# Kernel optimization log

Hardware: AMD Instinct MI355X
Metric: run time of the kernel (lower is better)

The kernel has to match this reference:

```python
import jax, jax.numpy as jnp
import numpy as np

V, Tb, D, H, L = 50257, 1024, 768, 12, 12
HS = D // H  # head size 64
DF = 4 * D   # MLP hidden 3072


def setup_inputs() -> dict:
    key = jax.random.key(0)
    ks = jax.random.split(key, 24)
    s = 0.02
    inp = {}
    inp['x'] = jax.random.randint(ks[0], (1, Tb), 0, V, dtype=jnp.int64)
    inp['wte'] = jax.random.normal(ks[1], (V, D), jnp.float32) * s
    inp['wpe'] = jax.random.normal(ks[2], (Tb, D), jnp.float32) * s
    # per-layer, per-head QKV linears, stacked: [L, H, D, HS]
    inp['Wq'] = jax.random.normal(ks[3], (L, H, D, HS), jnp.float32) * s
    inp['bq'] = jnp.zeros((L, H, HS), jnp.float32)
    inp['Wk'] = jax.random.normal(ks[4], (L, H, D, HS), jnp.float32) * s
    inp['bk'] = jnp.zeros((L, H, HS), jnp.float32)
    inp['Wv'] = jax.random.normal(ks[5], (L, H, D, HS), jnp.float32) * s
    inp['bv'] = jnp.zeros((L, H, HS), jnp.float32)
    inp['ln1_s'] = jnp.ones((L, D), jnp.float32)
    inp['ln1_b'] = jnp.zeros((L, D), jnp.float32)
    inp['W1'] = jax.random.normal(ks[6], (L, D, DF), jnp.float32) * s
    inp['b1'] = jnp.zeros((L, DF), jnp.float32)
    inp['W2'] = jax.random.normal(ks[7], (L, DF, D), jnp.float32) * s
    inp['b2'] = jnp.zeros((L, D), jnp.float32)
    inp['ln2_s'] = jnp.ones((L, D), jnp.float32)
    inp['ln2_b'] = jnp.zeros((L, D), jnp.float32)
    inp['lnf_s'] = jnp.ones((D,), jnp.float32)
    inp['lnf_b'] = jnp.zeros((D,), jnp.float32)
    inp['Wlm'] = jax.random.normal(ks[8], (D, V), jnp.float32) * s
    return inp


def _layernorm(x, scale, bias, eps=1e-5):
    mu = jnp.mean(x, axis=-1, keepdims=True)
    var = jnp.var(x, axis=-1, keepdims=True)
    return (x - mu) * jax.lax.rsqrt(var + eps) * scale + bias


def _gpt2_forward(x, wte, wpe, Wq, bq, Wk, bk, Wv, bv, ln1_s, ln1_b,
                  W1, b1, W2, b2, ln2_s, ln2_b, lnf_s, lnf_b, Wlm):
    B, T = x.shape
    h = wte[x] + wpe[jnp.arange(T)][None]  # [B, T, D]
    mask = jnp.tril(jnp.ones((T, T), jnp.bool_))
    for l in range(L):
        xn = _layernorm(h, ln1_s[l], ln1_b[l])
        # per-head linears, stacked -> [B, H, T, HS]
        q = jnp.einsum('btd,hde->bhte', xn, Wq[l]) + bq[l][None, :, None, :]
        k = jnp.einsum('btd,hde->bhte', xn, Wk[l]) + bk[l][None, :, None, :]
        v = jnp.einsum('btd,hde->bhte', xn, Wv[l]) + bv[l][None, :, None, :]
        # NOTE: original module does NOT scale scores by 1/sqrt(head_size)
        scores = jnp.einsum('bhte,bhse->bhts', q, k)
        scores = jnp.where(mask[None, None], scores, -jnp.inf)
        w = jax.nn.softmax(scores, axis=-1)
        attn = jnp.einsum('bhts,bhse->bhte', w, v)
        attn = attn.transpose(0, 2, 1, 3).reshape(B, T, H * HS)
        h = h + attn  # residual (no output projection in original)
        xn2 = _layernorm(h, ln2_s[l], ln2_b[l])
        mlp = jnp.einsum('btd,df->btf', xn2, W1[l]) + b1[l]
        mlp = jax.nn.gelu(mlp, approximate=False)  # nn.GELU default = exact
        mlp = jnp.einsum('btf,fd->btd', mlp, W2[l]) + b2[l]
        h = h + mlp
    h = _layernorm(h, lnf_s, lnf_b)
    logits = jnp.einsum('btd,dv->btv', h, Wlm)  # lm_head, no bias
    return logits


def reference(x, wte, wpe, Wq, bq, Wk, bk, Wv, bv, ln1_s, ln1_b,
              W1, b1, W2, b2, ln2_s, ln2_b, lnf_s, lnf_b, Wlm):
    return _gpt2_forward(x, wte, wpe, Wq, bq, Wk, bk, Wv, bv, ln1_s, ln1_b,
                         W1, b1, W2, b2, ln2_s, ln2_b, lnf_s, lnf_b, Wlm)
```

## Files before the change

### kernel.cpp

```cpp
#include <hip/hip_runtime.h>
#include <math.h>

#define TLEN 1024
#define DM   768
#define NH   12
#define HSZ  64
#define DF_  3072
#define NL   12
#define VC   50257
#define VCP  50304
#define NPAN (VCP/128)

typedef __attribute__((ext_vector_type(8))) short bf16x8;
typedef __attribute__((ext_vector_type(4))) float f32x4;

__device__ __forceinline__ float gelu_exact(float x){
  return 0.5f * x * (1.0f + erff(x * 0.70710678118654752f));
}
__device__ __forceinline__ short f2bf(float f){
  union { float f; unsigned u; } x; x.f = f;
  unsigned r = x.u + 0x7fffu + ((x.u >> 16) & 1u);
  return (short)(r >> 16);
}
__device__ __forceinline__ void gl16(const void* g, void* l){
  __builtin_amdgcn_global_load_lds(
      (const __attribute__((address_space(1))) unsigned int*)g,
      (__attribute__((address_space(3))) unsigned int*)l, 16, 0, 0);
}

__global__ __launch_bounds__(256) void embedln_k(const int* __restrict__ x,
    const float* __restrict__ wte, const float* __restrict__ wpe,
    const float* __restrict__ sc, const float* __restrict__ bi,
    float* __restrict__ h, short* __restrict__ out)
{
  int w = threadIdx.x >> 6, lane = threadIdx.x & 63;
  int t = blockIdx.x * 4 + w;
  int tok = x[t];
  size_t off = (size_t)t * DM;
  float v[12];
  float s = 0.f, s2 = 0.f;
  #pragma unroll
  for (int i = 0; i < 12; i++){
    int c = lane + i * 64;
    float xv = wte[(size_t)tok * DM + c] + wpe[off + c];
    h[off + c] = xv;
    v[i] = xv; s += xv; s2 += xv * xv;
  }
  #pragma unroll
  for (int o = 32; o; o >>= 1){ s += __shfl_xor(s, o); s2 += __shfl_xor(s2, o); }
  float mu = s * (1.0f / DM);
  float var = s2 * (1.0f / DM) - mu * mu;
  float rs = rsqrtf(var + 1e-5f);
  #pragma unroll
  for (int i = 0; i < 12; i++){
    int c = lane + i * 64;
    out[off + c] = f2bf((v[i] - mu) * rs * sc[c] + bi[c]);
  }
}

__global__ __launch_bounds__(256) void ln_k(const float* __restrict__ in,
    const float* __restrict__ sc, const float* __restrict__ bi,
    short* __restrict__ out)
{
  int w = threadIdx.x >> 6, lane = threadIdx.x & 63;
  int row = blockIdx.x * 4 + w;
  const float* r = in + (size_t)row * DM;
  float v[12];
  float s = 0.f, s2 = 0.f;
  #pragma unroll
  for (int i = 0; i < 12; i++){
    float xv = r[lane + i * 64];
    v[i] = xv; s += xv; s2 += xv * xv;
  }
  #pragma unroll
  for (int o = 32; o; o >>= 1){ s += __shfl_xor(s, o); s2 += __shfl_xor(s2, o); }
  float mu  = s * (1.0f / DM);
  float var = s2 * (1.0f / DM) - mu * mu;
  float rs  = rsqrtf(var + 1e-5f);
  short* o = out + (size_t)row * DM;
  #pragma unroll
  for (int i = 0; i < 12; i++){
    int c = lane + i * 64;
    o[c] = f2bf((v[i] - mu) * rs * sc[c] + bi[c]);
  }
}

__global__ __launch_bounds__(256) void redln_k(float* __restrict__ h,
    const float* __restrict__ p0, const float* __restrict__ p1,
    const float* __restrict__ bias,
    const float* __restrict__ sc, const float* __restrict__ bi,
    short* __restrict__ out)
{
  int w = threadIdx.x >> 6, lane = threadIdx.x & 63;
  int row = blockIdx.x * 4 + w;
  size_t off = (size_t)row * DM;
  float v[12];
  float s = 0.f, s2 = 0.f;
  #pragma unroll
  for (int i = 0; i < 12; i++){
    int c = lane + i * 64;
    float xv = h[off + c] + p0[off + c] + p1[off + c] + bias[c];
    h[off + c] = xv;
    v[i] = xv; s += xv; s2 += xv * xv;
  }
  #pragma unroll
  for (int o = 32; o; o >>= 1){ s += __shfl_xor(s, o); s2 += __shfl_xor(s2, o); }
  float mu  = s * (1.0f / DM);
  float var = s2 * (1.0f / DM) - mu * mu;
  float rs  = rsqrtf(var + 1e-5f);
  #pragma unroll
  for (int i = 0; i < 12; i++){
    int c = lane + i * 64;
    out[off + c] = f2bf((v[i] - mu) * rs * sc[c] + bi[c]);
  }
}

__global__ __launch_bounds__(256) void tc_k(const float* __restrict__ in,
    short* __restrict__ out, int K, int N, int ntiles, int per_mat,
    size_t in_stride, size_t out_stride)
{
  __shared__ short sh[64][65];
  int b = blockIdx.x;
  int l = b / per_mat, r = b - l * per_mat;
  int nt = r % ntiles, kt = r / ntiles;
  const float* ip = in + (size_t)l * in_stride;
  short* op = out + (size_t)l * out_stride;
  int n0 = nt * 64, k0 = kt * 64;
  int tid = threadIdx.x;
  if ((N & 3) == 0){
    #pragma unroll
    for (int it = 0; it < 4; it++){
      int idx = it * 256 + tid;
      int k = idx >> 4, n4 = (idx & 15) * 4;
      float4 v = *(const float4*)(ip + (size_t)(k0 + k) * N + n0 + n4);
      sh[k][n4+0] = f2bf(v.x); sh[k][n4+1] = f2bf(v.y);
      sh[k][n4+2] = f2bf(v.z); sh[k][n4+3] = f2bf(v.w);
    }
  } else {
    #pragma unroll
    for (int it = 0; it < 16; it++){
      int idx = it * 256 + tid;
      int k = idx >> 6, n = idx & 63;
      float v = (n0 + n < N) ? ip[(size_t)(k0 + k) * N + n0 + n] : 0.f;
      sh[k][n] = f2bf(v);
    }
  }
  __syncthreads();
  #pragma unroll
  for (int it = 0; it < 2; it++){
    int n = it * 32 + (tid >> 3);
    int kc = (tid & 7) * 8;
    bf16x8 v;
    #pragma unroll
    for (int u = 0; u < 8; u++) v[u] = sh[kc + u][n];
    *(bf16x8*)(op + (size_t)(n0 + n) * K + k0 + kc) = v;
  }
}

__global__ __launch_bounds__(256) void tcqkv_k(const float* __restrict__ Wq,
    const float* __restrict__ Wk, const float* __restrict__ Wv,
    short* __restrict__ out)
{
  __shared__ short sh[64][65];
  int b = blockIdx.x;
  int l = b / 144; int r = b - l * 144;
  int h = r / 12, kt = r - h * 12;
  int tid = threadIdx.x;
  for (int p = 0; p < 3; p++){
    const float* ip = (p == 0 ? Wq : p == 1 ? Wk : Wv)
                      + ((size_t)(l * NH + h) * DM + kt * 64) * 64;
    if (p) __syncthreads();
    #pragma unroll
    for (int it = 0; it < 4; it++){
      int idx = it * 256 + tid;
      int k = idx >> 4, e4 = (idx & 15) * 4;
      float4 v = *(const float4*)(ip + (size_t)k * 64 + e4);
      sh[k][e4+0] = f2bf(v.x); sh[k][e4+1] = f2bf(v.y);
      sh[k][e4+2] = f2bf(v.z); sh[k][e4+3] = f2bf(v.w);
    }
    __syncthreads();
    short* op = out + (size_t)l * 2304 * DM + (size_t)(p * DM + h * 64) * DM;
    #pragma unroll
    for (int it = 0; it < 2; it++){
      int e = it * 32 + (tid >> 3);
      int kc = (tid & 7) * 8;
      bf16x8 v;
      #pragma unroll
      for (int u = 0; u < 8; u++) v[u] = sh[kc + u][e];
      *(bf16x8*)(op + (size_t)e * DM + kt * 64 + kc) = v;
    }
  }
}

template<int MODE, int FI, int FJ>
__global__ __launch_bounds__(256) void mg_k(
    const short* __restrict__ A, const short* __restrict__ Bt,
    const float* __restrict__ b0, const float* __restrict__ b1,
    const float* __restrict__ b2,
    void* __restrict__ C0, void* __restrict__ C1, void* __restrict__ C2)
{
  constexpr int LDA    = (MODE == 2) ? DF_ : DM;
  constexpr int BM     = FI * 32;
  constexpr int BN     = FJ * 32;
  constexpr int ABYTES = BM * 64 * 2;
  constexpr int BBYTES = BN * 64 * 2;
  __shared__ __align__(16) char lds[2 * (ABYTES + BBYTES)];

  int tid = threadIdx.x;
  int wid = tid >> 6, lane = tid & 63;
  int l15 = lane & 15, l4 = lane >> 4;
  int wr = wid >> 1, wc = wid & 1;

  int m0, n0;
  if (MODE == 3){
    int xcd = blockIdx.x & 7, slot = blockIdx.x >> 3;
    int nb = xcd + 8 * (slot >> 3);
    if (nb >= NPAN) return;
    m0 = (slot & 7) * BM;
    n0 = nb * BN;
  } else {
    m0 = blockIdx.x * BM;
    n0 = blockIdx.y * BN;
  }
  int kbeg = (MODE == 2) ? blockIdx.z * (DF_ / 2) : 0;
  int nk   = ((MODE == 2) ? DF_ / 2 : LDA) / 64;

  f32x4 acc[FI][FJ] = {};
  int wbase = (tid & ~63) * 16;

  auto stage = [&](int k0, int b){
    char* ab = lds + b * ABYTES;
    char* bb = lds + 2 * ABYTES + b * BBYTES;
    #pragma unroll
    for (int ia = 0; ia < FI; ia++){
      int d = ia * 256 + tid;
      int row = d >> 3, gs = (d & 7) ^ (row & 7);
      gl16(A + (size_t)(m0 + row) * LDA + k0 + gs * 8, ab + ia * 4096 + wbase);
    }
    #pragma unroll
    for (int ib = 0; ib < FJ; ib++){
      int d = ib * 256 + tid;
      int row = d >> 3, gs = (d & 7) ^ (row & 7);
      gl16(Bt + (size_t)(n0 + row) * LDA + k0 + gs * 8, bb + ib * 4096 + wbase);
    }
  };

  stage(kbeg, 0);
  int cur = 0;
  for (int t = 0; t < nk; ++t){
    int k0 = kbeg + t * 64;
    if (t + 1 < nk){
      stage(k0 + 64, cur ^ 1);
      if constexpr (FI + FJ == 4) asm volatile("s_waitcnt vmcnt(4)" ::: "memory");
      else                        asm volatile("s_waitcnt vmcnt(8)" ::: "memory");
    } else {
      asm volatile("s_waitcnt vmcnt(0)" ::: "memory");
    }
    __builtin_amdgcn_s_barrier();
    __builtin_amdgcn_sched_barrier(0);

    char* ab = lds + cur * ABYTES;
    char* bb = lds + 2 * ABYTES + cur * BBYTES;
    #pragma unroll
    for (int kk = 0; kk < 2; kk++){
      bf16x8 af[FI], bfr[FJ];
      #pragma unroll
      for (int i = 0; i < FI; i++){
        int row = wr * (FI * 16) + i * 16 + l15;
        af[i] = *(const bf16x8*)(ab + row * 128 + (((kk * 4 + l4) ^ (row & 7)) * 16));
      }
      #pragma unroll
      for (int j = 0; j < FJ; j++){
        int row = wc * (FJ * 16) + j * 16 + l15;
        bfr[j] = *(const bf16x8*)(bb + row * 128 + (((kk * 4 + l4) ^ (row & 7)) * 16));
      }
      #pragma unroll
      for (int i = 0; i < FI; i++)
        #pragma unroll
        for (int j = 0; j < FJ; j++)
          acc[i][j] = __builtin_amdgcn_mfma_f32_16x16x32_bf16(af[i], bfr[j], acc[i][j], 0, 0, 0);
    }
    __builtin_amdgcn_sched_barrier(0);
    __builtin_amdgcn_s_barrier();
    cur ^= 1;
  }

  #pragma unroll
  for (int i = 0; i < FI; i++){
    int rowb = m0 + wr * (FI * 16) + i * 16 + l4 * 4;
    #pragma unroll
    for (int j = 0; j < FJ; j++){
      int col = n0 + wc * (FJ * 16) + j * 16 + l15;
      if (MODE == 0){
        int p = col / DM, within = col - p * DM;
        const float* bp = (p == 0) ? b0 : (p == 1) ? b1 : b2;
        float bb2 = bp[within];
        int hd = within >> 6, e = within & 63;
        if (p < 2){
          short* dst = (short*)((p == 0) ? C0 : C1);
          #pragma unroll
          for (int r = 0; r < 4; r++)
            dst[((size_t)hd * TLEN + rowb + r) * 64 + e] = f2bf(acc[i][j][r] + bb2);
        } else {
          short4 pk;
          pk.x = f2bf(acc[i][j][0] + bb2); pk.y = f2bf(acc[i][j][1] + bb2);
          pk.z = f2bf(acc[i][j][2] + bb2); pk.w = f2bf(acc[i][j][3] + bb2);
          *(short4*)((short*)C2 + ((size_t)hd * 64 + e) * TLEN + rowb) = pk;
        }
      } else if (MODE == 1){
        #pragma unroll
        for (int r = 0; r < 4; r++)
          ((short*)C0)[(size_t)(rowb + r) * DF_ + col] =
              f2bf(gelu_exact(acc[i][j][r] + b0[col]));
      } else if (MODE == 2){
        float* dst = (float*)((blockIdx.z == 0) ? C0 : C1);
        #pragma unroll
        for (int r = 0; r < 4; r++)
          dst[(size_t)(rowb + r) * DM + col] = acc[i][j][r];
      } else {
        if (col < VC){
          #pragma unroll
          for (int r = 0; r < 4; r++)
            ((float*)C0)[(size_t)(rowb + r) * VC + col] = acc[i][j][r];
        }
      }
    }
  }
}

__global__ __launch_bounds__(256) void attn_k(const short* __restrict__ q,
    const short* __restrict__ k, const short* __restrict__ vt,
    float* __restrict__ h)
{
  __shared__ short P_lds[4][16][72];
  int tid = threadIdx.x;
  int wid = tid >> 6, lane = tid & 63;
  int l15 = lane & 15, l4 = lane >> 4;
  int head = blockIdx.x >> 4, qt = blockIdx.x & 15;
  int qb = qt * 64 + wid * 16;

  const short* qh = q  + (size_t)head * TLEN * 64;
  const short* kh = k  + (size_t)head * TLEN * 64;
  const short* vh = vt + (size_t)head * 64 * TLEN;

  bf16x8 qf[2];
  qf[0] = *(const bf16x8*)(qh + (size_t)(qb + l15) * 64 + l4 * 8);
  qf[1] = *(const bf16x8*)(qh + (size_t)(qb + l15) * 64 + 32 + l4 * 8);

  f32x4 O[4] = {};
  float mrow[4] = {-3e38f, -3e38f, -3e38f, -3e38f};
  float lrow[4] = {0.f, 0.f, 0.f, 0.f};

  for (int kv0 = 0; kv0 <= qb + 15; kv0 += 64){
    f32x4 S[4] = {};
    #pragma unroll
    for (int kk = 0; kk < 2; kk++){
      #pragma unroll
      for (int j = 0; j < 4; j++){
        bf16x8 kf = *(const bf16x8*)(kh + (size_t)(kv0 + j*16 + l15) * 64
                                     + kk*32 + l4*8);
        S[j] = __builtin_amdgcn_mfma_f32_16x16x32_bf16(qf[kk], kf, S[j], 0, 0, 0);
      }
    }
    if (kv0 + 63 > qb){
      #pragma unroll
      for (int j = 0; j < 4; j++){
        int kvc = kv0 + j*16 + l15;
        #pragma unroll
        for (int r = 0; r < 4; r++)
          if (kvc > qb + l4*4 + r) S[j][r] = -3e38f;
      }
    }
    #pragma unroll
    for (int r = 0; r < 4; r++){
      float mx = fmaxf(fmaxf(S[0][r], S[1][r]), fmaxf(S[2][r], S[3][r]));
      #pragma unroll
      for (int off = 1; off < 16; off <<= 1) mx = fmaxf(mx, __shfl_xor(mx, off));
      float mn = fmaxf(mrow[r], mx);
      float corr = __expf(mrow[r] - mn);
      mrow[r] = mn;
      float sm = 0.f;
      #pragma unroll
      for (int j = 0; j < 4; j++){
        float p = __expf(S[j][r] - mn);
        S[j][r] = p; sm += p;
      }
      #pragma unroll
      for (int off = 1; off < 16; off <<= 1) sm += __shfl_xor(sm, off);
      lrow[r] = lrow[r] * corr + sm;
      #pragma unroll
      for (int j = 0; j < 4; j++) O[j][r] *= corr;
    }
    #pragma unroll
    for (int j = 0; j < 4; j++)
      #pragma unroll
      for (int r = 0; r < 4; r++)
        P_lds[wid][l4*4 + r][j*16 + l15] = f2bf(S[j][r]);
    #pragma unroll
    for (int kk = 0; kk < 2; kk++){
      bf16x8 pa = *(const bf16x8*)(&P_lds[wid][l15][kk*32 + l4*8]);
      #pragma unroll
      for (int jd = 0; jd < 4; jd++){
        bf16x8 vf = *(const bf16x8*)(vh + (size_t)(jd*16 + l15) * TLEN
                                     + kv0 + kk*32 + l4*8);
        O[jd] = __builtin_amdgcn_mfma_f32_16x16x32_bf16(pa, vf, O[jd], 0, 0, 0);
      }
    }
  }

  #pragma unroll
  for (int r = 0; r < 4; r++){
    float inv = 1.0f / lrow[r];
    int t = qb + l4*4 + r;
    #pragma unroll
    for (int jd = 0; jd < 4; jd++){
      int d = head * 64 + jd*16 + l15;
      h[(size_t)t * DM + d] += O[jd][r] * inv;
    }
  }
}

extern "C" void kernel_launch(void* const* d_in, const int* in_sizes, int n_in,
                              void* d_out, int out_size, void* d_ws, size_t ws_size,
                              hipStream_t stream)
{
  const int*   x    = (const int*)  d_in[0];
  const float* wte  = (const float*)d_in[1];
  const float* wpe  = (const float*)d_in[2];
  const float* Wq   = (const float*)d_in[3];
  const float* bq   = (const float*)d_in[4];
  const float* Wk   = (const float*)d_in[5];
  const float* bk   = (const float*)d_in[6];
  const float* Wv   = (const float*)d_in[7];
  const float* bv   = (const float*)d_in[8];
  const float* ln1s = (const float*)d_in[9];
  const float* ln1b = (const float*)d_in[10];
  const float* W1   = (const float*)d_in[11];
  const float* b1   = (const float*)d_in[12];
  const float* W2   = (const float*)d_in[13];
  const float* b2   = (const float*)d_in[14];
  const float* ln2s = (const float*)d_in[15];
  const float* ln2b = (const float*)d_in[16];
  const float* lnfs = (const float*)d_in[17];
  const float* lnfb = (const float*)d_in[18];
  const float* Wlm  = (const float*)d_in[19];
  float* out = (float*)d_out;

  const size_t SZ_QKVT = (size_t)NL * 2304 * DM * 2;
  const size_t SZ_W1T  = (size_t)NL * DF_ * DM * 2;
  const size_t SZ_W2T  = (size_t)NL * DM * DF_ * 2;
  const size_t SZ_WLMT = (size_t)VCP * DM * 2;
  const size_t SZ_H    = (size_t)TLEN * DM * 4;
  const size_t SZ_BF   = (size_t)TLEN * DM * 2;

  char* ws = (char*)d_ws;
  short* wqkvT = (short*)ws;  ws += SZ_QKVT;
  short* w1T   = (short*)ws;  ws += SZ_W1T;
  short* w2T   = (short*)ws;  ws += SZ_W2T;
  short* wlmT  = (short*)ws;  ws += SZ_WLMT;
  float* h     = (float*)ws;  ws += SZ_H;
  short* qb    = (short*)ws;  ws += SZ_BF;
  short* kb    = (short*)ws;  ws += SZ_BF;
  short* vtb   = (short*)ws;  ws += SZ_BF;
  short* xnb   = (short*)ws;  ws += SZ_BF;
  short* mhb   = (short*)ws;  ws += (size_t)TLEN * DF_ * 2;
  float* p1    = (float*)ws;
  float* p0    = (float*)qb;

  tcqkv_k<<<NL*NH*12, 256, 0, stream>>>(Wq, Wk, Wv, wqkvT);
  tc_k<<<NL*48*12, 256, 0, stream>>>(W1, w1T, DM, DF_, 48, 576,
                                     (size_t)DM*DF_, (size_t)DM*DF_);
  tc_k<<<NL*12*48, 256, 0, stream>>>(W2, w2T, DF_, DM, 12, 576,
                                     (size_t)DM*DF_, (size_t)DM*DF_);
  tc_k<<<786*12, 256, 0, stream>>>(Wlm, wlmT, DM, VC, 786, 786*12, 0, 0);

  embedln_k<<<TLEN/4, 256, 0, stream>>>(x, wte, wpe, ln1s, ln1b, h, xnb);

  for (int l = 0; l < NL; ++l){
    mg_k<0,2,2><<<dim3(16,36), 256, 0, stream>>>(xnb, wqkvT + (size_t)l*2304*DM,
        bq + l*DM, bk + l*DM, bv + l*DM, qb, kb, vtb);
    attn_k<<<NH*16, 256, 0, stream>>>(qb, kb, vtb, h);
    ln_k<<<TLEN/4, 256, 0, stream>>>(h, ln2s + l*DM, ln2b + l*DM, xnb);
    mg_k<1,2,2><<<dim3(16,48), 256, 0, stream>>>(xnb, w1T + (size_t)l*DF_*DM,
        b1 + l*DF_, nullptr, nullptr, mhb, nullptr, nullptr);
    mg_k<2,2,2><<<dim3(16,12,2), 256, 0, stream>>>(mhb, w2T + (size_t)l*DM*DF_,
        nullptr, nullptr, nullptr, p0, p1, nullptr);
    const float* nsc = (l < NL-1) ? ln1s + (l+1)*DM : lnfs;
    const float* nbi = (l < NL-1) ? ln1b + (l+1)*DM : lnfb;
    redln_k<<<TLEN/4, 256, 0, stream>>>(h, p0, p1, b2 + l*DM, nsc, nbi, xnb);
  }

  mg_k<3,4,4><<<3200, 256, 0, stream>>>(xnb, wlmT,
      nullptr, nullptr, nullptr, out, nullptr, nullptr);
}
```

Before: 1.316 ms.

## Load GEMM A fragments directly from global into registers, stage only B in LDS

The GEMM kernel stops staging the A tile through shared memory. Each wave now loads its A fragments straight from global memory into registers, double-buffered across k-steps, and only the B tile stays in LDS. The main loop is unrolled by two with explicit vmcnt waits sized to the new load count. This cuts LDS traffic and footprint, which can help occupancy. The cost is uncoalesced, duplicated A loads across waves (both wc waves fetch the same rows), higher register pressure, and a wait count that must match exactly. The loop also assumes nk is even.

```diff
diff --git a/kernel.cpp b/kernel.cpp
--- a/kernel.cpp
+++ b/kernel.cpp
@@ -9,7 +9,6 @@
 #define NL   12
 #define VC   50257
 #define VCP  50304
-#define NPAN (VCP/128)
 
 typedef __attribute__((ext_vector_type(8))) short bf16x8;
 typedef __attribute__((ext_vector_type(4))) float f32x4;
@@ -202,9 +201,9 @@
   constexpr int LDA    = (MODE == 2) ? DF_ : DM;
   constexpr int BM     = FI * 32;
   constexpr int BN     = FJ * 32;
-  constexpr int ABYTES = BM * 64 * 2;
   constexpr int BBYTES = BN * 64 * 2;
-  __shared__ __align__(16) char lds[2 * (ABYTES + BBYTES)];
+  constexpr int W      = FJ + 2 * FI;
+  __shared__ __align__(16) char lds[2 * BBYTES];
 
   int tid = threadIdx.x;
   int wid = tid >> 6, lane = tid & 63;
@@ -213,9 +212,10 @@
 
   int m0, n0;
   if (MODE == 3){
+    constexpr int npan = VCP / BN;
     int xcd = blockIdx.x & 7, slot = blockIdx.x >> 3;
     int nb = xcd + 8 * (slot >> 3);
-    if (nb >= NPAN) return;
+    if (nb >= npan) return;
     m0 = (slot & 7) * BM;
     n0 = nb * BN;
   } else {
@@ -223,20 +223,14 @@
     n0 = blockIdx.y * BN;
   }
   int kbeg = (MODE == 2) ? blockIdx.z * (DF_ / 2) : 0;
-  int nk   = ((MODE == 2) ? DF_ / 2 : LDA) / 64;
+  const int nk = ((MODE == 2) ? DF_ / 2 : LDA) / 64;
 
   f32x4 acc[FI][FJ] = {};
   int wbase = (tid & ~63) * 16;
-
-  auto stage = [&](int k0, int b){
-    char* ab = lds + b * ABYTES;
-    char* bb = lds + 2 * ABYTES + b * BBYTES;
-    #pragma unroll
-    for (int ia = 0; ia < FI; ia++){
-      int d = ia * 256 + tid;
-      int row = d >> 3, gs = (d & 7) ^ (row & 7);
-      gl16(A + (size_t)(m0 + row) * LDA + k0 + gs * 8, ab + ia * 4096 + wbase);
-    }
+  const short* Ab = A + (size_t)(m0 + wr * (FI * 16) + l15) * LDA + l4 * 8;
+
+  auto stageB = [&](int k0, int b){
+    char* bb = lds + b * BBYTES;
     #pragma unroll
     for (int ib = 0; ib < FJ; ib++){
       int d = ib * 256 + tid;
@@ -244,31 +238,18 @@
       gl16(Bt + (size_t)(n0 + row) * LDA + k0 + gs * 8, bb + ib * 4096 + wbase);
     }
   };
-
-  stage(kbeg, 0);
-  int cur = 0;
-  for (int t = 0; t < nk; ++t){
-    int k0 = kbeg + t * 64;
-    if (t + 1 < nk){
-      stage(k0 + 64, cur ^ 1);
-      if constexpr (FI + FJ == 4) asm volatile("s_waitcnt vmcnt(4)" ::: "memory");
-      else                        asm volatile("s_waitcnt vmcnt(8)" ::: "memory");
-    } else {
-      asm volatile("s_waitcnt vmcnt(0)" ::: "memory");
-    }
-    __builtin_amdgcn_s_barrier();
-    __builtin_amdgcn_sched_barrier(0);
-
-    char* ab = lds + cur * ABYTES;
-    char* bb = lds + 2 * ABYTES + cur * BBYTES;
+  auto loadA = [&](int k0, bf16x8 (&a)[2][FI]){
+    #pragma unroll
+    for (int kk = 0; kk < 2; kk++)
+      #pragma unroll
+      for (int i = 0; i < FI; i++)
+        a[kk][i] = *(const bf16x8*)(Ab + (size_t)i * 16 * LDA + k0 + kk * 32);
+  };
+  auto compute = [&](int b, bf16x8 (&a)[2][FI]){
+    char* bb = lds + b * BBYTES;
     #pragma unroll
     for (int kk = 0; kk < 2; kk++){
-      bf16x8 af[FI], bfr[FJ];
-      #pragma unroll
-      for (int i = 0; i < FI; i++){
-        int row = wr * (FI * 16) + i * 16 + l15;
-        af[i] = *(const bf16x8*)(ab + row * 128 + (((kk * 4 + l4) ^ (row & 7)) * 16));
-      }
+      bf16x8 bfr[FJ];
       #pragma unroll
       for (int j = 0; j < FJ; j++){
         int row = wc * (FJ * 16) + j * 16 + l15;
@@ -278,11 +259,41 @@
       for (int i = 0; i < FI; i++)
         #pragma unroll
         for (int j = 0; j < FJ; j++)
-          acc[i][j] = __builtin_amdgcn_mfma_f32_16x16x32_bf16(af[i], bfr[j], acc[i][j], 0, 0, 0);
-    }
-    __builtin_amdgcn_sched_barrier(0);
-    __builtin_amdgcn_s_barrier();
-    cur ^= 1;
+          acc[i][j] = __builtin_amdgcn_mfma_f32_16x16x32_bf16(a[kk][i], bfr[j], acc[i][j], 0, 0, 0);
+    }
+  };
+
+  bf16x8 aC[2][FI], aN[2][FI];
+  stageB(kbeg, 0);
+  loadA(kbeg, aC);
+
+  for (int t = 0; t < nk; t += 2){
+    {
+      stageB(kbeg + (t + 1) * 64, 1);
+      loadA(kbeg + (t + 1) * 64, aN);
+      if constexpr (W == 6)  asm volatile("s_waitcnt vmcnt(6)"  ::: "memory");
+      else                   asm volatile("s_waitcnt vmcnt(12)" ::: "memory");
+      __builtin_amdgcn_s_barrier();
+      __builtin_amdgcn_sched_barrier(0);
+      compute(0, aC);
+      __builtin_amdgcn_sched_barrier(0);
+      __builtin_amdgcn_s_barrier();
+    }
+    {
+      if (t + 2 < nk){
+        stageB(kbeg + (t + 2) * 64, 0);
+        loadA(kbeg + (t + 2) * 64, aC);
+        if constexpr (W == 6)  asm volatile("s_waitcnt vmcnt(6)"  ::: "memory");
+        else                   asm volatile("s_waitcnt vmcnt(12)" ::: "memory");
+      } else {
+        asm volatile("s_waitcnt vmcnt(0)" ::: "memory");
+      }
+      __builtin_amdgcn_s_barrier();
+      __builtin_amdgcn_sched_barrier(0);
+      compute(1, aN);
+      __builtin_amdgcn_sched_barrier(0);
+      __builtin_amdgcn_s_barrier();
+    }
   }
 
   #pragma unroll
```

New measurement: 1.751 ms. 33.0% more time.

## Replace LM-head GEMM launch with persistent-style kernel looping over panels

Applied to the files above, without the earlier changes.

The LM-head GEMM moves from a 3200-block launch of the generic templated kernel to a dedicated 512-block kernel. Each block keeps a fixed 128-row M slot and loops over up to seven N panels, with XCD-aware panel assignment. This is meant to cut block launch and tail overhead and keep each XCD working on nearby weight panels for cache reuse. The cost is that the first K-tile load of each new panel is no longer overlapped with the previous panel's epilogue, and load balance across blocks may be uneven.

```diff
diff --git a/kernel.cpp b/kernel.cpp
--- a/kernel.cpp
+++ b/kernel.cpp
@@ -9,7 +9,7 @@
 #define NL   12
 #define VC   50257
 #define VCP  50304
-#define NPAN (VCP/128)
+#define NPAN128 393
 
 typedef __attribute__((ext_vector_type(8))) short bf16x8;
 typedef __attribute__((ext_vector_type(4))) float f32x4;
@@ -211,17 +211,8 @@
   int l15 = lane & 15, l4 = lane >> 4;
   int wr = wid >> 1, wc = wid & 1;
 
-  int m0, n0;
-  if (MODE == 3){
-    int xcd = blockIdx.x & 7, slot = blockIdx.x >> 3;
-    int nb = xcd + 8 * (slot >> 3);
-    if (nb >= NPAN) return;
-    m0 = (slot & 7) * BM;
-    n0 = nb * BN;
-  } else {
-    m0 = blockIdx.x * BM;
-    n0 = blockIdx.y * BN;
-  }
+  int m0 = blockIdx.x * BM;
+  int n0 = blockIdx.y * BN;
   int kbeg = (MODE == 2) ? blockIdx.z * (DF_ / 2) : 0;
   int nk   = ((MODE == 2) ? DF_ / 2 : LDA) / 64;
 
@@ -317,14 +308,105 @@
         #pragma unroll
         for (int r = 0; r < 4; r++)
           dst[(size_t)(rowb + r) * DM + col] = acc[i][j][r];
+      }
+    }
+  }
+}
+
+__global__ __launch_bounds__(256) void lm_k(const short* __restrict__ A,
+    const short* __restrict__ Bt, float* __restrict__ C)
+{
+  constexpr int ABYTES = 128 * 64 * 2;
+  constexpr int BBYTES = 128 * 64 * 2;
+  __shared__ __align__(16) char lds[2 * (ABYTES + BBYTES)];
+
+  int tid = threadIdx.x;
+  int wid = tid >> 6, lane = tid & 63;
+  int l15 = lane & 15, l4 = lane >> 4;
+  int wr = wid >> 1, wc = wid & 1;
+  int wbase = (tid & ~63) * 16;
+
+  int xcd = blockIdx.x & 7, mslot = (blockIdx.x >> 3) & 7, g = blockIdx.x >> 6;
+  int m0 = mslot * 128;
+
+  int n0;
+  auto stage = [&](int k0, int b){
+    char* ab = lds + b * ABYTES;
+    char* bb = lds + 2 * ABYTES + b * BBYTES;
+    #pragma unroll
+    for (int ia = 0; ia < 4; ia++){
+      int d = ia * 256 + tid;
+      int row = d >> 3, gs = (d & 7) ^ (row & 7);
+      gl16(A + (size_t)(m0 + row) * DM + k0 + gs * 8, ab + ia * 4096 + wbase);
+    }
+    #pragma unroll
+    for (int ib = 0; ib < 4; ib++){
+      int d = ib * 256 + tid;
+      int row = d >> 3, gs = (d & 7) ^ (row & 7);
+      gl16(Bt + (size_t)(n0 + row) * DM + k0 + gs * 8, bb + ib * 4096 + wbase);
+    }
+  };
+
+  int nb = xcd + 8 * (g * 7);
+  if (nb >= NPAN128) return;
+  n0 = nb * 128;
+  stage(0, 0);
+
+  for (int p = 0; ; ){
+    f32x4 acc[4][4] = {};
+    int cur = 0;
+    for (int t = 0; t < 12; ++t){
+      if (t + 1 < 12){
+        stage(t * 64 + 64, cur ^ 1);
+        asm volatile("s_waitcnt vmcnt(8)" ::: "memory");
       } else {
+        asm volatile("s_waitcnt vmcnt(0)" ::: "memory");
+      }
+      __builtin_amdgcn_s_barrier();
+      __builtin_amdgcn_sched_barrier(0);
+      char* ab = lds + cur * ABYTES;
+      char* bb = lds + 2 * ABYTES + cur * BBYTES;
+      #pragma unroll
+      for (int kk = 0; kk < 2; kk++){
+        bf16x8 af[4], bfr[4];
+        #pragma unroll
+        for (int i = 0; i < 4; i++){
+          int row = wr * 64 + i * 16 + l15;
+          af[i] = *(const bf16x8*)(ab + row * 128 + (((kk * 4 + l4) ^ (row & 7)) * 16));
+        }
+        #pragma unroll
+        for (int j = 0; j < 4; j++){
+          int row = wc * 64 + j * 16 + l15;
+          bfr[j] = *(const bf16x8*)(bb + row * 128 + (((kk * 4 + l4) ^ (row & 7)) * 16));
+        }
+        #pragma unroll
+        for (int i = 0; i < 4; i++)
+          #pragma unroll
+          for (int j = 0; j < 4; j++)
+            acc[i][j] = __builtin_amdgcn_mfma_f32_16x16x32_bf16(af[i], bfr[j], acc[i][j], 0, 0, 0);
+      }
+      __builtin_amdgcn_sched_barrier(0);
+      __builtin_amdgcn_s_barrier();
+      cur ^= 1;
+    }
+    #pragma unroll
+    for (int i = 0; i < 4; i++){
+      int rowb = m0 + wr * 64 + i * 16 + l4 * 4;
+      #pragma unroll
+      for (int j = 0; j < 4; j++){
+        int col = n0 + wc * 64 + j * 16 + l15;
         if (col < VC){
           #pragma unroll
           for (int r = 0; r < 4; r++)
-            ((float*)C0)[(size_t)(rowb + r) * VC + col] = acc[i][j][r];
+            C[(size_t)(rowb + r) * VC + col] = acc[i][j][r];
         }
       }
     }
+    p++;
+    int nbn = xcd + 8 * (g * 7 + p);
+    if (p >= 7 || nbn >= NPAN128) break;
+    n0 = nbn * 128;
+    stage(0, 0);
   }
 }
 
@@ -490,6 +572,5 @@
     redln_k<<<TLEN/4, 256, 0, stream>>>(h, p0, p1, b2 + l*DM, nsc, nbi, xnb);
   }
 
-  mg_k<3,4,4><<<3200, 256, 0, stream>>>(xnb, wlmT,
-      nullptr, nullptr, nullptr, out, nullptr, nullptr);
-}
+  lm_k<<<512, 256, 0, stream>>>(xnb, wlmT, out);
+}
```

Result: slower. 1.353 ms (+2.8%).
